# Optimization experiments

Measured on AMD Instinct MI355X. Metric: run time of the kernel, lower is better.

## Reference

```python
import jax, jax.numpy as jnp
import numpy as np

SEQ, B, IN, H = 512, 64, 1024, 1024

def _lstm_layer(x_seq, Wx, bx, Wh, bh):
    # x_seq: [S, B, D], Wx: [4H, D], Wh: [4H, H]
    h0 = jnp.zeros((x_seq.shape[1], Wh.shape[1]), x_seq.dtype)
    c0 = jnp.zeros_like(h0)
    def step(carry, x_t):
        h, c = carry
        z = x_t @ Wx.T + bx + h @ Wh.T + bh  # [B, 4H]
        i, f, g, o = jnp.split(z, 4, axis=1)
        c1 = jax.nn.sigmoid(f) * c + jax.nn.sigmoid(i) * jnp.tanh(g)
        h1 = jax.nn.sigmoid(o) * jnp.tanh(c1)
        return (h1, c1), h1
    _, hs = jax.lax.scan(step, (h0, c0), x_seq)
    return hs  # [S, B, H]

def setup_inputs() -> dict:
    key = jax.random.key(0)
    ks = jax.random.split(key, 9)
    s_in = 1.0 / np.sqrt(IN)
    s_h = 1.0 / np.sqrt(H)
    return {
        "x": jax.random.normal(ks[0], (SEQ, B, IN), jnp.float32),
        "Wx0": jax.random.uniform(ks[1], (4 * H, IN), jnp.float32, -s_in, s_in),
        "bx0": jax.random.uniform(ks[2], (4 * H,), jnp.float32, -s_in, s_in),
        "Wh0": jax.random.uniform(ks[3], (4 * H, H), jnp.float32, -s_h, s_h),
        "bh0": jax.random.uniform(ks[4], (4 * H,), jnp.float32, -s_h, s_h),
        "Wx1": jax.random.uniform(ks[5], (4 * H, H), jnp.float32, -s_h, s_h),
        "bx1": jax.random.uniform(ks[6], (4 * H,), jnp.float32, -s_h, s_h),
        "Wh1": jax.random.uniform(ks[7], (4 * H, H), jnp.float32, -s_h, s_h),
        "bh1": jax.random.uniform(ks[8], (4 * H,), jnp.float32, -s_h, s_h),
    }

def reference(x, Wx0, bx0, Wh0, bh0, Wx1, bx1, Wh1, bh1):
    # Two stacked unidirectional LSTM layers, zero initial states.
    h_seq0 = _lstm_layer(x, Wx0, bx0, Wh0, bh0)
    h_seq1 = _lstm_layer(h_seq0, Wx1, bx1, Wh1, bh1)
    return h_seq1  # [S, B, H] = stacked version of the torch list output
```

## Files before the change

kernel.cpp:

```cpp
#include <hip/hip_runtime.h>


#define SEQ   512
#define BATCH 64
#define HID   1024
#define NG    4096
#define KCAT  2048
#define F0_BASE 0
#define E0_IDX  8192
#define F1_BASE 16384
#define E1_IDX  24576

#define SMEM_BYTES 133504

typedef __attribute__((ext_vector_type(8))) _Float16 f16x8;
typedef __attribute__((ext_vector_type(4))) _Float16 f16x4;
typedef __attribute__((ext_vector_type(4))) float    f32x4;

__device__ __forceinline__ float sigm_f(float x){ return 1.f/(1.f + __expf(-x)); }
__device__ __forceinline__ float tanh_f(float x){
    float e = __expf(-2.f*fabsf(x));
    float r = (1.f - e)/(1.f + e);
    return copysignf(r, x);
}

__device__ __forceinline__ void store_h8(_Float16* p, f16x4 v){
    asm volatile("global_store_dwordx2 %0, %1, off sc0 sc1" :: "v"(p), "v"(v) : "memory");
}
__device__ __forceinline__ void drain_vmem(){
    asm volatile("s_waitcnt vmcnt(0)" ::: "memory");
}


__global__ void prep_w_kernel(const float* __restrict__ Wx, const float* __restrict__ Wh,
                              const float* __restrict__ bx, const float* __restrict__ bh,
                              _Float16* __restrict__ Wr, float* __restrict__ br){
    int p = blockIdx.x;
    int j = p >> 2, g = p & 3;
    int r = g*1024 + j;
    int k = threadIdx.x * 8;
    const float* s = (k < 1024) ? (Wx + (size_t)r*1024 + k)
                                : (Wh + (size_t)r*1024 + (k - 1024));
    float4 v0 = *reinterpret_cast<const float4*>(s);
    float4 v1 = *reinterpret_cast<const float4*>(s + 4);
    f16x8 o;
    o[0]=(_Float16)v0.x; o[1]=(_Float16)v0.y; o[2]=(_Float16)v0.z; o[3]=(_Float16)v0.w;
    o[4]=(_Float16)v1.x; o[5]=(_Float16)v1.y; o[6]=(_Float16)v1.z; o[7]=(_Float16)v1.w;
    *reinterpret_cast<f16x8*>(Wr + (size_t)p*KCAT + k) = o;
    if (threadIdx.x == 0) br[p] = bx[r] + bh[r];
}

__global__ void prep_x_kernel(const float* __restrict__ x, _Float16* xo){
    size_t i = ((size_t)blockIdx.x*256 + threadIdx.x) * 8;
    float4 v0 = *reinterpret_cast<const float4*>(x + i);
    float4 v1 = *reinterpret_cast<const float4*>(x + i + 4);
    f16x8 o;
    o[0]=(_Float16)v0.x; o[1]=(_Float16)v0.y; o[2]=(_Float16)v0.z; o[3]=(_Float16)v0.w;
    o[4]=(_Float16)v1.x; o[5]=(_Float16)v1.y; o[6]=(_Float16)v1.z; o[7]=(_Float16)v1.w;
    *reinterpret_cast<f16x8*>(xo + i) = o;
}

__global__ void init_misc_kernel(int* flags, _Float16* hz){
    int i = blockIdx.x*256 + threadIdx.x;
    flags[i] = 0;
    if (i < 16384){
        f16x4 z; z[0]=(_Float16)0.f; z[1]=(_Float16)0.f; z[2]=(_Float16)0.f; z[3]=(_Float16)0.f;
        *reinterpret_cast<f16x4*>(hz + (size_t)i*4) = z;
    }
}


__device__ __forceinline__ void wait_epoch_g(const int* flags, int eidx, int k, int rep){
    for(;;){
        int e = __hip_atomic_load(&flags[eidx + rep*32], __ATOMIC_RELAXED, __HIP_MEMORY_SCOPE_AGENT);
        if (e >= k) break;
        __builtin_amdgcn_s_sleep(2);
    }
    asm volatile("" ::: "memory");
}

__device__ __forceinline__ void aggregate_publish(int* flags, int base, int eidx,
                                                  int k, int lane){
    const int b = lane*4;
    for(;;){
        int a0 = __hip_atomic_load(&flags[base + (b+0)*32], __ATOMIC_RELAXED, __HIP_MEMORY_SCOPE_AGENT);
        int a1 = __hip_atomic_load(&flags[base + (b+1)*32], __ATOMIC_RELAXED, __HIP_MEMORY_SCOPE_AGENT);
        int a2 = __hip_atomic_load(&flags[base + (b+2)*32], __ATOMIC_RELAXED, __HIP_MEMORY_SCOPE_AGENT);
        int a3 = __hip_atomic_load(&flags[base + (b+3)*32], __ATOMIC_RELAXED, __HIP_MEMORY_SCOPE_AGENT);
        bool ok = (a0>=k) && (a1>=k) && (a2>=k) && (a3>=k);
        if (__all(ok)) break;
        __builtin_amdgcn_s_sleep(1);
    }
    asm volatile("" ::: "memory");
    if (lane < 8)
        __hip_atomic_store(&flags[eidx + lane*32], k, __ATOMIC_RELAXED, __HIP_MEMORY_SCOPE_AGENT);
}

__device__ __forceinline__ void lds_publish(int* e, int k){
    __hip_atomic_store(e, k, __ATOMIC_RELAXED, __HIP_MEMORY_SCOPE_WORKGROUP);
}
__device__ __forceinline__ void lds_wait(int* e, int k){
    while (__hip_atomic_load(e, __ATOMIC_RELAXED, __HIP_MEMORY_SCOPE_WORKGROUP) < k)
        __builtin_amdgcn_s_sleep(1);
    asm volatile("" ::: "memory");
}


__device__ __forceinline__ f32x4 mfma16(f16x8 a, f16x8 b, f32x4 c){
    return __builtin_amdgcn_mfma_f32_16x16x32_f16(a, b, c, 0, 0, 0);
}

__device__ __forceinline__ void gemm_pipe_ldsb(const _Float16* A, const char* wrow,
                                               int c0, int swz, f32x4* acc){
    f16x8 abuf[2][16];
    #pragma unroll
    for (int kk = 0; kk < 4; ++kk)
        #pragma unroll
        for (int m = 0; m < 4; ++m)
            abuf[0][kk*4+m] = *reinterpret_cast<const f16x8*>(A + kk*32 + m*16*1024);
    #pragma unroll
    for (int b = 0; b < 4; ++b){
        if (b < 3){
            #pragma unroll
            for (int kk = 0; kk < 4; ++kk)
                #pragma unroll
                for (int m = 0; m < 4; ++m)
                    abuf[(b+1)&1][kk*4+m] =
                        *reinterpret_cast<const f16x8*>(A + (b+1)*128 + kk*32 + m*16*1024);
        }
        #pragma unroll
        for (int kk = 0; kk < 4; ++kk){
            const int kg = b*4 + kk;
            f16x8 bb = *reinterpret_cast<const f16x8*>(wrow + ((c0 + kg*64) ^ swz));
            acc[0] = mfma16(abuf[b&1][kk*4+0], bb, acc[0]);
            acc[1] = mfma16(abuf[b&1][kk*4+1], bb, acc[1]);
            acc[2] = mfma16(abuf[b&1][kk*4+2], bb, acc[2]);
            acc[3] = mfma16(abuf[b&1][kk*4+3], bb, acc[3]);
        }
    }
}

__device__ __forceinline__ void gemm_pipe_gb(const _Float16* A, const _Float16* Wp,
                                             f32x4* acc){
    f16x8 abuf[2][16];
    #pragma unroll
    for (int kk = 0; kk < 4; ++kk)
        #pragma unroll
        for (int m = 0; m < 4; ++m)
            abuf[0][kk*4+m] = *reinterpret_cast<const f16x8*>(A + kk*32 + m*16*1024);
    #pragma unroll
    for (int b = 0; b < 4; ++b){
        if (b < 3){
            #pragma unroll
            for (int kk = 0; kk < 4; ++kk)
                #pragma unroll
                for (int m = 0; m < 4; ++m)
                    abuf[(b+1)&1][kk*4+m] =
                        *reinterpret_cast<const f16x8*>(A + (b+1)*128 + kk*32 + m*16*1024);
        }
        #pragma unroll
        for (int kk = 0; kk < 4; ++kk){
            const int kg = b*4 + kk;
            f16x8 bb = *reinterpret_cast<const f16x8*>(Wp + kg*32);
            acc[0] = mfma16(abuf[b&1][kk*4+0], bb, acc[0]);
            acc[1] = mfma16(abuf[b&1][kk*4+1], bb, acc[1]);
            acc[2] = mfma16(abuf[b&1][kk*4+2], bb, acc[2]);
            acc[3] = mfma16(abuf[b&1][kk*4+3], bb, acc[3]);
        }
    }
}

__device__ __forceinline__ void gemm_q_f32(const float* A, const _Float16* Wp, f32x4* acc){
    #pragma unroll 2
    for (int kk = 0; kk < 16; ++kk){
        f16x8 b = *reinterpret_cast<const f16x8*>(Wp + kk*32);
        f16x8 a[4];
        #pragma unroll
        for (int m = 0; m < 4; ++m){
            float4 u0 = *reinterpret_cast<const float4*>(A + kk*32 + (size_t)m*16*1024);
            float4 u1 = *reinterpret_cast<const float4*>(A + kk*32 + (size_t)m*16*1024 + 4);
            f16x8 v;
            v[0]=(_Float16)u0.x; v[1]=(_Float16)u0.y; v[2]=(_Float16)u0.z; v[3]=(_Float16)u0.w;
            v[4]=(_Float16)u1.x; v[5]=(_Float16)u1.y; v[6]=(_Float16)u1.z; v[7]=(_Float16)u1.w;
            a[m] = v;
        }
        acc[0] = mfma16(a[0], b, acc[0]);
        acc[1] = mfma16(a[1], b, acc[1]);
        acc[2] = mfma16(a[2], b, acc[2]);
        acc[3] = mfma16(a[3], b, acc[3]);
    }
}


__global__ __launch_bounds__(256, 1)
void lstm_persist(const _Float16* __restrict__ Wr0, const _Float16* __restrict__ Wr1,
                  const float* __restrict__ br0, const float* __restrict__ br1,
                  const _Float16* __restrict__ xbf, const float* __restrict__ xf32,
                  int use_xf16, const _Float16* __restrict__ hz,
                  _Float16* h0ring, _Float16* h1ring, float* out, int* flags){
    extern __shared__ char smem[];
    float (*accL)[4][64][17] = reinterpret_cast<float(*)[4][64][17]>(smem + 98304);
    int* ldsE = reinterpret_cast<int*>(smem + 133120);

    const int tid  = threadIdx.x;
    const int wg   = blockIdx.x;
    const int wv   = tid >> 6;
    const int lane = tid & 63;
    const int r    = lane & 15;
    const int q    = lane >> 4;
    const int p0   = wg * 16;
    const int rep  = wg & 7;
    const int swz  = (r & 7) << 4;

    for (int idx = tid; idx < 6144; idx += 256){
        int rr, cb; char* dst; const _Float16* s;
        if (idx < 2048){
            rr = idx >> 7;  cb = (idx & 127) << 4;
            s   = Wr0 + (size_t)(p0 + rr)*KCAT + 1024 + (cb >> 1);
            dst = smem + rr*2048 + (cb ^ ((rr & 7) << 4));
        } else {
            int j2 = idx - 2048;
            rr = j2 >> 8;  cb = (j2 & 255) << 4;
            s   = Wr1 + (size_t)(p0 + rr)*KCAT + (cb >> 1);
            dst = smem + 32768 + rr*4096 + (cb ^ ((rr & 7) << 4));
        }
        *reinterpret_cast<f16x8*>(dst) = *reinterpret_cast<const f16x8*>(s);
    }
    if (tid == 0) *ldsE = 0;
    __syncthreads();

    f32x4 cst = {0.f,0.f,0.f,0.f};
    f32x4 ho_keep = {0.f,0.f,0.f,0.f};
    f32x4 bias[4];
    {
        const float* bsrc = (wv == 0) ? br0 : br1;
        #pragma unroll
        for (int jj = 0; jj < 4; ++jj)
            bias[jj] = *reinterpret_cast<const f32x4*>(&bsrc[p0 + jj*4]);
    }

    const int kofs = (wv & 1)*512 + q*8;
    const int wcol = wv*512 + q*8;
    const char* w1row  = smem + 32768 + r*4096;
    const char* wh0row = smem + r*2048;
    const size_t BH = (size_t)BATCH*HID;

    for (int k = 0; k <= SEQ; ++k){
        f32x4 acc[4];
        #pragma unroll
        for (int m = 0; m < 4; ++m){ acc[m].x=0;acc[m].y=0;acc[m].z=0;acc[m].w=0; }

        if (wv < 2){
            if (k < SEQ){
                if (use_xf16)
                    gemm_pipe_gb(xbf + (size_t)k*BH + (size_t)r*HID + kofs,
                                 Wr0 + (size_t)(p0 + r)*KCAT + wcol, acc);
                else
                    gemm_q_f32(xf32 + (size_t)k*BH + (size_t)r*HID + kofs,
                               Wr0 + (size_t)(p0 + r)*KCAT + wcol, acc);
            }
        } else {
            if (k > 0){
                if (wv == 3){
                    if (wg == 0) aggregate_publish(flags, F0_BASE, E0_IDX, k, lane);
                    else         wait_epoch_g(flags, E0_IDX, k, rep);
                    lds_publish(ldsE, k);
                } else {
                    lds_wait(ldsE, k);
                }
            }
            if (k < SEQ){
                const _Float16* A0 = (k == 0) ? (hz + (size_t)r*HID + kofs)
                                              : (h0ring + (size_t)(k-1)*BH + (size_t)r*HID + kofs);
                gemm_pipe_ldsb(A0, wh0row, (wv-2)*1024 + q*16, swz, acc);
            }
        }

        #pragma unroll
        for (int mt = 0; mt < 4; ++mt)
            #pragma unroll
            for (int j = 0; j < 4; ++j)
                accL[0][wv][mt*16 + q*4 + j][r] = acc[mt][j];
        __syncthreads();

        if (wv == 0 && k < SEQ){
            f32x4 zz[4];
            #pragma unroll
            for (int jj = 0; jj < 4; ++jj) zz[jj] = bias[jj];
            #pragma unroll
            for (int w2 = 0; w2 < 4; ++w2)
                #pragma unroll
                for (int jj = 0; jj < 4; ++jj){
                    f32x4 a = *reinterpret_cast<const f32x4*>(&accL[0][w2][lane][jj*4]);
                    zz[jj].x += a.x; zz[jj].y += a.y; zz[jj].z += a.z; zz[jj].w += a.w;
                }
            f16x4 hv;
            #pragma unroll
            for (int jl = 0; jl < 4; ++jl){
                float ig = sigm_f(zz[jl].x), fg = sigm_f(zz[jl].y);
                float gg = tanh_f(zz[jl].z), og = sigm_f(zz[jl].w);
                float c = fg*cst[jl] + ig*gg;  cst[jl] = c;
                hv[jl] = (_Float16)(og * tanh_f(c));
            }
            store_h8(h0ring + ((size_t)k*BATCH + lane)*HID + wg*4, hv);
            drain_vmem();
            if (lane == 0)
                __hip_atomic_store(&flags[F0_BASE + wg*32], k + 1,
                                   __ATOMIC_RELAXED, __HIP_MEMORY_SCOPE_AGENT);
        }

        #pragma unroll
        for (int m = 0; m < 4; ++m){ acc[m].x=0;acc[m].y=0;acc[m].z=0;acc[m].w=0; }

        if (k >= 1){
            if (wv < 2){
                gemm_pipe_ldsb(h0ring + (size_t)(k-1)*BH + (size_t)r*HID + kofs,
                               w1row, wv*1024 + q*16, swz, acc);
            } else {
                if (k >= 2){
                    if (wg == 0 && wv == 2) aggregate_publish(flags, F1_BASE, E1_IDX, k-1, lane);
                    else                    wait_epoch_g(flags, E1_IDX, k-1, rep);
                }
                const _Float16* A1 = (k == 1) ? (hz + (size_t)r*HID + kofs)
                                              : (h1ring + (size_t)(k-2)*BH + (size_t)r*HID + kofs);
                gemm_pipe_ldsb(A1, w1row, wv*1024 + q*16, swz, acc);
            }
        }

        #pragma unroll
        for (int mt = 0; mt < 4; ++mt)
            #pragma unroll
            for (int j = 0; j < 4; ++j)
                accL[1][wv][mt*16 + q*4 + j][r] = acc[mt][j];
        __syncthreads();

        if (wv == 1 && k >= 1){
            const int t1 = k - 1;
            f32x4 zz[4];
            #pragma unroll
            for (int jj = 0; jj < 4; ++jj) zz[jj] = bias[jj];
            #pragma unroll
            for (int w2 = 0; w2 < 4; ++w2)
                #pragma unroll
                for (int jj = 0; jj < 4; ++jj){
                    f32x4 a = *reinterpret_cast<const f32x4*>(&accL[1][w2][lane][jj*4]);
                    zz[jj].x += a.x; zz[jj].y += a.y; zz[jj].z += a.z; zz[jj].w += a.w;
                }
            f16x4 hv; f32x4 ho;
            #pragma unroll
            for (int jl = 0; jl < 4; ++jl){
                float ig = sigm_f(zz[jl].x), fg = sigm_f(zz[jl].y);
                float gg = tanh_f(zz[jl].z), og = sigm_f(zz[jl].w);
                float c = fg*cst[jl] + ig*gg;  cst[jl] = c;
                float h = og * tanh_f(c);
                hv[jl] = (_Float16)h;  ho[jl] = h;
            }
            if (k < SEQ) store_h8(h1ring + ((size_t)t1*BATCH + lane)*HID + wg*4, hv);
            if (t1 < SEQ-1) *reinterpret_cast<f32x4*>(out + ((size_t)t1*BATCH + lane)*HID + wg*4) = ho;
            else            ho_keep = ho;
            drain_vmem();
            if (lane == 0)
                __hip_atomic_store(&flags[F1_BASE + wg*32], k,
                                   __ATOMIC_RELAXED, __HIP_MEMORY_SCOPE_AGENT);
        }
    }

    if (tid == 0)
        __hip_atomic_store(&flags[F0_BASE + wg*32], SEQ + 1,
                           __ATOMIC_RELAXED, __HIP_MEMORY_SCOPE_AGENT);
    if (wg == 0 && wv == 3) aggregate_publish(flags, F0_BASE, E0_IDX, SEQ + 1, lane);
    if (wv == 1){
        wait_epoch_g(flags, E0_IDX, SEQ + 1, rep);
        *reinterpret_cast<f32x4*>(out + ((size_t)(SEQ-1)*BATCH + lane)*HID + wg*4) = ho_keep;
    }
}


extern "C" void kernel_launch(void* const* d_in, const int* in_sizes, int n_in,
                              void* d_out, int out_size, void* d_ws, size_t ws_size,
                              hipStream_t stream){
    const float* x   = (const float*)d_in[0];
    const float* Wx0 = (const float*)d_in[1];
    const float* bx0 = (const float*)d_in[2];
    const float* Wh0 = (const float*)d_in[3];
    const float* bh0 = (const float*)d_in[4];
    const float* Wx1 = (const float*)d_in[5];
    const float* bx1 = (const float*)d_in[6];
    const float* Wh1 = (const float*)d_in[7];
    const float* bh1 = (const float*)d_in[8];
    float* out = (float*)d_out;
    char* ws = (char*)d_ws;

    size_t o = 0;
    _Float16* Wr0 = (_Float16*)(ws + o); o += (size_t)NG*KCAT*2;
    _Float16* Wr1 = (_Float16*)(ws + o); o += (size_t)NG*KCAT*2;
    float* br0 = (float*)(ws + o); o += 16384;
    float* br1 = (float*)(ws + o); o += 16384;
    _Float16* h1ring = (_Float16*)(ws + o); o += (size_t)SEQ*BATCH*HID*2;
    _Float16* hz     = (_Float16*)(ws + o); o += (size_t)BATCH*HID*2;
    int* flags = (int*)(ws + o); o += 131072;

    const size_t RING = (size_t)SEQ*BATCH*HID*2;
    _Float16 *xbf = nullptr, *h0ring;
    int use_xf16 = 0;
    if (ws_size >= o + 2*RING){
        xbf    = (_Float16*)(ws + o);  o += RING;  use_xf16 = 1;
        h0ring = (_Float16*)(ws + o);  o += RING;
    } else if (ws_size >= o + RING){
        xbf    = (_Float16*)(ws + o);  o += RING;  use_xf16 = 1;
        h0ring = (_Float16*)((char*)d_out + (size_t)64*1024*1024);
    } else {
        h0ring = (_Float16*)((char*)d_out + (size_t)64*1024*1024);
    }

    hipFuncSetAttribute((const void*)lstm_persist,
                        hipFuncAttributeMaxDynamicSharedMemorySize, SMEM_BYTES);

    prep_w_kernel<<<NG, 256, 0, stream>>>(Wx0, Wh0, bx0, bh0, Wr0, br0);
    prep_w_kernel<<<NG, 256, 0, stream>>>(Wx1, Wh1, bx1, bh1, Wr1, br1);
    if (use_xf16)
        prep_x_kernel<<<(SEQ*BATCH*HID)/(256*8), 256, 0, stream>>>(x, xbf);
    init_misc_kernel<<<128, 256, 0, stream>>>(flags, hz);
    lstm_persist<<<256, 256, SMEM_BYTES, stream>>>(Wr0, Wr1, br0, br1, xbf, x, use_xf16,
                                                   hz, h0ring, h1ring, out, flags);
}
```

Measured before the change: 8.843 ms.

## Add dedicated sync wave per block and replace syncthreads with counter barrier

```diff
diff --git a/kernel.cpp b/kernel.cpp
--- a/kernel.cpp
+++ b/kernel.cpp
@@ -11,7 +11,7 @@
 #define F1_BASE 16384
 #define E1_IDX  24576
 
-#define SMEM_BYTES 133504
+#define SMEM_BYTES 133184
 
 typedef __attribute__((ext_vector_type(8))) _Float16 f16x8;
 typedef __attribute__((ext_vector_type(4))) _Float16 f16x4;
@@ -70,38 +70,31 @@
 }
 
 
-__device__ __forceinline__ void wait_epoch_g(const int* flags, int eidx, int k, int rep){
-    for(;;){
-        int e = __hip_atomic_load(&flags[eidx + rep*32], __ATOMIC_RELAXED, __HIP_MEMORY_SCOPE_AGENT);
-        if (e >= k) break;
-        __builtin_amdgcn_s_sleep(2);
-    }
-    asm volatile("" ::: "memory");
-}
-
-__device__ __forceinline__ void aggregate_publish(int* flags, int base, int eidx,
-                                                  int k, int lane){
-    const int b = lane*4;
-    for(;;){
-        int a0 = __hip_atomic_load(&flags[base + (b+0)*32], __ATOMIC_RELAXED, __HIP_MEMORY_SCOPE_AGENT);
-        int a1 = __hip_atomic_load(&flags[base + (b+1)*32], __ATOMIC_RELAXED, __HIP_MEMORY_SCOPE_AGENT);
-        int a2 = __hip_atomic_load(&flags[base + (b+2)*32], __ATOMIC_RELAXED, __HIP_MEMORY_SCOPE_AGENT);
-        int a3 = __hip_atomic_load(&flags[base + (b+3)*32], __ATOMIC_RELAXED, __HIP_MEMORY_SCOPE_AGENT);
-        bool ok = (a0>=k) && (a1>=k) && (a2>=k) && (a3>=k);
-        if (__all(ok)) break;
-        __builtin_amdgcn_s_sleep(1);
-    }
-    asm volatile("" ::: "memory");
-    if (lane < 8)
-        __hip_atomic_store(&flags[eidx + lane*32], k, __ATOMIC_RELAXED, __HIP_MEMORY_SCOPE_AGENT);
-}
-
-__device__ __forceinline__ void lds_publish(int* e, int k){
-    __hip_atomic_store(e, k, __ATOMIC_RELAXED, __HIP_MEMORY_SCOPE_WORKGROUP);
-}
-__device__ __forceinline__ void lds_wait(int* e, int k){
+__device__ __forceinline__ int gload(const int* p){
+    return __hip_atomic_load(p, __ATOMIC_RELAXED, __HIP_MEMORY_SCOPE_AGENT);
+}
+__device__ __forceinline__ void gstore(int* p, int v){
+    __hip_atomic_store(p, v, __ATOMIC_RELAXED, __HIP_MEMORY_SCOPE_AGENT);
+}
+__device__ __forceinline__ void lstore(int* p, int v){
+    __hip_atomic_store(p, v, __ATOMIC_RELAXED, __HIP_MEMORY_SCOPE_WORKGROUP);
+}
+__device__ __forceinline__ void lds_wait(const int* e, int k){
     while (__hip_atomic_load(e, __ATOMIC_RELAXED, __HIP_MEMORY_SCOPE_WORKGROUP) < k)
         __builtin_amdgcn_s_sleep(1);
+    asm volatile("" ::: "memory");
+}
+__device__ __forceinline__ int wave_min(int v){
+    #pragma unroll
+    for (int off = 1; off < 64; off <<= 1)
+        v = min(v, __shfl_xor(v, off));
+    return v;
+}
+__device__ __forceinline__ void bar4(int* cnt, int target){
+    asm volatile("s_waitcnt lgkmcnt(0)" ::: "memory");
+    if ((threadIdx.x & 63) == 0)
+        __hip_atomic_fetch_add(cnt, 1, __ATOMIC_RELAXED, __HIP_MEMORY_SCOPE_WORKGROUP);
+    while (__hip_atomic_load(cnt, __ATOMIC_RELAXED, __HIP_MEMORY_SCOPE_WORKGROUP) < target) {}
     asm volatile("" ::: "memory");
 }
 
@@ -192,7 +185,7 @@
 }
 
 
-__global__ __launch_bounds__(256, 1)
+__global__ __launch_bounds__(320, 1)
 void lstm_persist(const _Float16* __restrict__ Wr0, const _Float16* __restrict__ Wr1,
                   const float* __restrict__ br0, const float* __restrict__ br1,
                   const _Float16* __restrict__ xbf, const float* __restrict__ xf32,
@@ -200,7 +193,9 @@
                   _Float16* h0ring, _Float16* h1ring, float* out, int* flags){
     extern __shared__ char smem[];
     float (*accL)[4][64][17] = reinterpret_cast<float(*)[4][64][17]>(smem + 98304);
-    int* ldsE = reinterpret_cast<int*>(smem + 133120);
+    int* ldsE0  = reinterpret_cast<int*>(smem + 133120);
+    int* ldsE1  = reinterpret_cast<int*>(smem + 133124);
+    int* barCnt = reinterpret_cast<int*>(smem + 133128);
 
     const int tid  = threadIdx.x;
     const int wg   = blockIdx.x;
@@ -209,10 +204,9 @@
     const int r    = lane & 15;
     const int q    = lane >> 4;
     const int p0   = wg * 16;
-    const int rep  = wg & 7;
     const int swz  = (r & 7) << 4;
 
-    for (int idx = tid; idx < 6144; idx += 256){
+    for (int idx = tid; idx < 6144; idx += 320){
         int rr, cb; char* dst; const _Float16* s;
         if (idx < 2048){
             rr = idx >> 7;  cb = (idx & 127) << 4;
@@ -226,8 +220,47 @@
         }
         *reinterpret_cast<f16x8*>(dst) = *reinterpret_cast<const f16x8*>(s);
     }
-    if (tid == 0) *ldsE = 0;
+    if (tid == 0){ *ldsE0 = 0; *ldsE1 = 0; *barCnt = 0; }
     __syncthreads();
+
+    if (wv == 4){
+        int e0 = 0, e1 = 0;
+        if (wg == 0){
+            for(;;){
+                int f0 = 0x7fffffff, f1 = 0x7fffffff;
+                #pragma unroll
+                for (int j = 0; j < 4; ++j){
+                    int i4 = lane*4 + j;
+                    f0 = min(f0, gload(&flags[F0_BASE + i4*32]));
+                    f1 = min(f1, gload(&flags[F1_BASE + i4*32]));
+                }
+                int g0 = wave_min(f0), g1 = wave_min(f1);
+                if (g0 > e0){
+                    if (lane < 32) gstore(&flags[E0_IDX + lane*32], g0);
+                    if (lane == 0) lstore(ldsE0, g0);
+                    e0 = g0;
+                }
+                if (g1 > e1){
+                    if (lane < 32) gstore(&flags[E1_IDX + lane*32], g1);
+                    if (lane == 0) lstore(ldsE1, g1);
+                    e1 = g1;
+                }
+                if (e1 >= SEQ) break;
+                __builtin_amdgcn_s_sleep(1);
+            }
+        } else {
+            const int ri = (wg & 31)*32;
+            for(;;){
+                int v0 = gload(&flags[E0_IDX + ri]);
+                int v1 = gload(&flags[E1_IDX + ri]);
+                if (v0 > e0){ if (lane == 0) lstore(ldsE0, v0); e0 = v0; }
+                if (v1 > e1){ if (lane == 0) lstore(ldsE1, v1); e1 = v1; }
+                if (e1 >= SEQ) break;
+                __builtin_amdgcn_s_sleep(1);
+            }
+        }
+        return;
+    }
 
     f32x4 cst = {0.f,0.f,0.f,0.f};
     f32x4 ho_keep = {0.f,0.f,0.f,0.f};
@@ -244,6 +277,7 @@
     const char* w1row  = smem + 32768 + r*4096;
     const char* wh0row = smem + r*2048;
     const size_t BH = (size_t)BATCH*HID;
+    int btgt = 4;
 
     for (int k = 0; k <= SEQ; ++k){
         f32x4 acc[4];
@@ -260,15 +294,7 @@
                                Wr0 + (size_t)(p0 + r)*KCAT + wcol, acc);
             }
         } else {
-            if (k > 0){
-                if (wv == 3){
-                    if (wg == 0) aggregate_publish(flags, F0_BASE, E0_IDX, k, lane);
-                    else         wait_epoch_g(flags, E0_IDX, k, rep);
-                    lds_publish(ldsE, k);
-                } else {
-                    lds_wait(ldsE, k);
-                }
-            }
+            if (k > 0) lds_wait(ldsE0, k);
             if (k < SEQ){
                 const _Float16* A0 = (k == 0) ? (hz + (size_t)r*HID + kofs)
                                               : (h0ring + (size_t)(k-1)*BH + (size_t)r*HID + kofs);
@@ -281,7 +307,7 @@
             #pragma unroll
             for (int j = 0; j < 4; ++j)
                 accL[0][wv][mt*16 + q*4 + j][r] = acc[mt][j];
-        __syncthreads();
+        bar4(barCnt, btgt); btgt += 4;
 
         if (wv == 0 && k < SEQ){
             f32x4 zz[4];
@@ -304,9 +330,7 @@
             }
             store_h8(h0ring + ((size_t)k*BATCH + lane)*HID + wg*4, hv);
             drain_vmem();
-            if (lane == 0)
-                __hip_atomic_store(&flags[F0_BASE + wg*32], k + 1,
-                                   __ATOMIC_RELAXED, __HIP_MEMORY_SCOPE_AGENT);
+            if (lane == 0) gstore(&flags[F0_BASE + wg*32], k + 1);
         }
 
         #pragma unroll
@@ -314,13 +338,11 @@
 
         if (k >= 1){
             if (wv < 2){
+                lds_wait(ldsE0, k);
                 gemm_pipe_ldsb(h0ring + (size_t)(k-1)*BH + (size_t)r*HID + kofs,
                                w1row, wv*1024 + q*16, swz, acc);
             } else {
-                if (k >= 2){
-                    if (wg == 0 && wv == 2) aggregate_publish(flags, F1_BASE, E1_IDX, k-1, lane);
-                    else                    wait_epoch_g(flags, E1_IDX, k-1, rep);
-                }
+                if (k >= 2) lds_wait(ldsE1, k-1);
                 const _Float16* A1 = (k == 1) ? (hz + (size_t)r*HID + kofs)
                                               : (h1ring + (size_t)(k-2)*BH + (size_t)r*HID + kofs);
                 gemm_pipe_ldsb(A1, w1row, wv*1024 + q*16, swz, acc);
@@ -332,7 +354,7 @@
             #pragma unroll
             for (int j = 0; j < 4; ++j)
                 accL[1][wv][mt*16 + q*4 + j][r] = acc[mt][j];
-        __syncthreads();
+        bar4(barCnt, btgt); btgt += 4;
 
         if (wv == 1 && k >= 1){
             const int t1 = k - 1;
@@ -359,18 +381,12 @@
             if (t1 < SEQ-1) *reinterpret_cast<f32x4*>(out + ((size_t)t1*BATCH + lane)*HID + wg*4) = ho;
             else            ho_keep = ho;
             drain_vmem();
-            if (lane == 0)
-                __hip_atomic_store(&flags[F1_BASE + wg*32], k,
-                                   __ATOMIC_RELAXED, __HIP_MEMORY_SCOPE_AGENT);
-        }
-    }
-
-    if (tid == 0)
-        __hip_atomic_store(&flags[F0_BASE + wg*32], SEQ + 1,
-                           __ATOMIC_RELAXED, __HIP_MEMORY_SCOPE_AGENT);
-    if (wg == 0 && wv == 3) aggregate_publish(flags, F0_BASE, E0_IDX, SEQ + 1, lane);
+            if (lane == 0) gstore(&flags[F1_BASE + wg*32], k);
+        }
+    }
+
     if (wv == 1){
-        wait_epoch_g(flags, E0_IDX, SEQ + 1, rep);
+        lds_wait(ldsE1, SEQ);
         *reinterpret_cast<f32x4*>(out + ((size_t)(SEQ-1)*BATCH + lane)*HID + wg*4) = ho_keep;
     }
 }
@@ -421,6 +437,6 @@
     if (use_xf16)
         prep_x_kernel<<<(SEQ*BATCH*HID)/(256*8), 256, 0, stream>>>(x, xbf);
     init_misc_kernel<<<128, 256, 0, stream>>>(flags, hz);
-    lstm_persist<<<256, 256, SMEM_BYTES, stream>>>(Wr0, Wr1, br0, br1, xbf, x, use_xf16,
+    lstm_persist<<<256, 320, SMEM_BYTES, stream>>>(Wr0, Wr1, br0, br1, xbf, x, use_xf16,
                                                    hz, h0ring, h1ring, out, flags);
 }
```

Measured after the change: 12.51 ms. 1.41x slower.

## Restructure epoch sync: more flag replicas, eager aggregation, simpler GEMM loads

Applied to the files above, without the earlier changes.

```diff
diff --git a/kernel.cpp b/kernel.cpp
--- a/kernel.cpp
+++ b/kernel.cpp
@@ -92,17 +92,8 @@
         __builtin_amdgcn_s_sleep(1);
     }
     asm volatile("" ::: "memory");
-    if (lane < 8)
+    if (lane < 32)
         __hip_atomic_store(&flags[eidx + lane*32], k, __ATOMIC_RELAXED, __HIP_MEMORY_SCOPE_AGENT);
-}
-
-__device__ __forceinline__ void lds_publish(int* e, int k){
-    __hip_atomic_store(e, k, __ATOMIC_RELAXED, __HIP_MEMORY_SCOPE_WORKGROUP);
-}
-__device__ __forceinline__ void lds_wait(int* e, int k){
-    while (__hip_atomic_load(e, __ATOMIC_RELAXED, __HIP_MEMORY_SCOPE_WORKGROUP) < k)
-        __builtin_amdgcn_s_sleep(1);
-    asm volatile("" ::: "memory");
 }
 
 
@@ -110,63 +101,65 @@
     return __builtin_amdgcn_mfma_f32_16x16x32_f16(a, b, c, 0, 0, 0);
 }
 
-__device__ __forceinline__ void gemm_pipe_ldsb(const _Float16* A, const char* wrow,
+__device__ __forceinline__ void gemm_half_ldsb(const _Float16* A, const char* wrow,
                                                int c0, int swz, f32x4* acc){
-    f16x8 abuf[2][16];
-    #pragma unroll
-    for (int kk = 0; kk < 4; ++kk)
+    f16x8 a[32];
+    #pragma unroll
+    for (int kk = 0; kk < 8; ++kk)
         #pragma unroll
         for (int m = 0; m < 4; ++m)
-            abuf[0][kk*4+m] = *reinterpret_cast<const f16x8*>(A + kk*32 + m*16*1024);
-    #pragma unroll
-    for (int b = 0; b < 4; ++b){
-        if (b < 3){
-            #pragma unroll
-            for (int kk = 0; kk < 4; ++kk)
-                #pragma unroll
-                for (int m = 0; m < 4; ++m)
-                    abuf[(b+1)&1][kk*4+m] =
-                        *reinterpret_cast<const f16x8*>(A + (b+1)*128 + kk*32 + m*16*1024);
-        }
-        #pragma unroll
-        for (int kk = 0; kk < 4; ++kk){
-            const int kg = b*4 + kk;
-            f16x8 bb = *reinterpret_cast<const f16x8*>(wrow + ((c0 + kg*64) ^ swz));
-            acc[0] = mfma16(abuf[b&1][kk*4+0], bb, acc[0]);
-            acc[1] = mfma16(abuf[b&1][kk*4+1], bb, acc[1]);
-            acc[2] = mfma16(abuf[b&1][kk*4+2], bb, acc[2]);
-            acc[3] = mfma16(abuf[b&1][kk*4+3], bb, acc[3]);
-        }
-    }
-}
-
-__device__ __forceinline__ void gemm_pipe_gb(const _Float16* A, const _Float16* Wp,
+            a[kk*4+m] = *reinterpret_cast<const f16x8*>(A + kk*32 + m*16*1024);
+    #pragma unroll
+    for (int kk = 0; kk < 8; ++kk){
+        f16x8 bb = *reinterpret_cast<const f16x8*>(wrow + ((c0 + kk*64) ^ swz));
+        acc[0] = mfma16(a[kk*4+0], bb, acc[0]);
+        acc[1] = mfma16(a[kk*4+1], bb, acc[1]);
+        acc[2] = mfma16(a[kk*4+2], bb, acc[2]);
+        acc[3] = mfma16(a[kk*4+3], bb, acc[3]);
+    }
+    #pragma unroll
+    for (int kk = 8; kk < 16; ++kk)
+        #pragma unroll
+        for (int m = 0; m < 4; ++m)
+            a[(kk-8)*4+m] = *reinterpret_cast<const f16x8*>(A + kk*32 + m*16*1024);
+    #pragma unroll
+    for (int kk = 8; kk < 16; ++kk){
+        f16x8 bb = *reinterpret_cast<const f16x8*>(wrow + ((c0 + kk*64) ^ swz));
+        acc[0] = mfma16(a[(kk-8)*4+0], bb, acc[0]);
+        acc[1] = mfma16(a[(kk-8)*4+1], bb, acc[1]);
+        acc[2] = mfma16(a[(kk-8)*4+2], bb, acc[2]);
+        acc[3] = mfma16(a[(kk-8)*4+3], bb, acc[3]);
+    }
+}
+
+__device__ __forceinline__ void gemm_half_gb(const _Float16* A, const _Float16* Wp,
                                              f32x4* acc){
-    f16x8 abuf[2][16];
-    #pragma unroll
-    for (int kk = 0; kk < 4; ++kk)
+    f16x8 a[32];
+    #pragma unroll
+    for (int kk = 0; kk < 8; ++kk)
         #pragma unroll
         for (int m = 0; m < 4; ++m)
-            abuf[0][kk*4+m] = *reinterpret_cast<const f16x8*>(A + kk*32 + m*16*1024);
-    #pragma unroll
-    for (int b = 0; b < 4; ++b){
-        if (b < 3){
-            #pragma unroll
-            for (int kk = 0; kk < 4; ++kk)
-                #pragma unroll
-                for (int m = 0; m < 4; ++m)
-                    abuf[(b+1)&1][kk*4+m] =
-                        *reinterpret_cast<const f16x8*>(A + (b+1)*128 + kk*32 + m*16*1024);
-        }
-        #pragma unroll
-        for (int kk = 0; kk < 4; ++kk){
-            const int kg = b*4 + kk;
-            f16x8 bb = *reinterpret_cast<const f16x8*>(Wp + kg*32);
-            acc[0] = mfma16(abuf[b&1][kk*4+0], bb, acc[0]);
-            acc[1] = mfma16(abuf[b&1][kk*4+1], bb, acc[1]);
-            acc[2] = mfma16(abuf[b&1][kk*4+2], bb, acc[2]);
-            acc[3] = mfma16(abuf[b&1][kk*4+3], bb, acc[3]);
-        }
+            a[kk*4+m] = *reinterpret_cast<const f16x8*>(A + kk*32 + m*16*1024);
+    #pragma unroll
+    for (int kk = 0; kk < 8; ++kk){
+        f16x8 bb = *reinterpret_cast<const f16x8*>(Wp + kk*32);
+        acc[0] = mfma16(a[kk*4+0], bb, acc[0]);
+        acc[1] = mfma16(a[kk*4+1], bb, acc[1]);
+        acc[2] = mfma16(a[kk*4+2], bb, acc[2]);
+        acc[3] = mfma16(a[kk*4+3], bb, acc[3]);
+    }
+    #pragma unroll
+    for (int kk = 8; kk < 16; ++kk)
+        #pragma unroll
+        for (int m = 0; m < 4; ++m)
+            a[(kk-8)*4+m] = *reinterpret_cast<const f16x8*>(A + kk*32 + m*16*1024);
+    #pragma unroll
+    for (int kk = 8; kk < 16; ++kk){
+        f16x8 bb = *reinterpret_cast<const f16x8*>(Wp + kk*32);
+        acc[0] = mfma16(a[(kk-8)*4+0], bb, acc[0]);
+        acc[1] = mfma16(a[(kk-8)*4+1], bb, acc[1]);
+        acc[2] = mfma16(a[(kk-8)*4+2], bb, acc[2]);
+        acc[3] = mfma16(a[(kk-8)*4+3], bb, acc[3]);
     }
 }
 
@@ -200,7 +193,6 @@
                   _Float16* h0ring, _Float16* h1ring, float* out, int* flags){
     extern __shared__ char smem[];
     float (*accL)[4][64][17] = reinterpret_cast<float(*)[4][64][17]>(smem + 98304);
-    int* ldsE = reinterpret_cast<int*>(smem + 133120);
 
     const int tid  = threadIdx.x;
     const int wg   = blockIdx.x;
@@ -209,7 +201,7 @@
     const int r    = lane & 15;
     const int q    = lane >> 4;
     const int p0   = wg * 16;
-    const int rep  = wg & 7;
+    const int rep  = wg & 31;
     const int swz  = (r & 7) << 4;
 
     for (int idx = tid; idx < 6144; idx += 256){
@@ -226,7 +218,6 @@
         }
         *reinterpret_cast<f16x8*>(dst) = *reinterpret_cast<const f16x8*>(s);
     }
-    if (tid == 0) *ldsE = 0;
     __syncthreads();
 
     f32x4 cst = {0.f,0.f,0.f,0.f};
@@ -253,26 +244,18 @@
         if (wv < 2){
             if (k < SEQ){
                 if (use_xf16)
-                    gemm_pipe_gb(xbf + (size_t)k*BH + (size_t)r*HID + kofs,
+                    gemm_half_gb(xbf + (size_t)k*BH + (size_t)r*HID + kofs,
                                  Wr0 + (size_t)(p0 + r)*KCAT + wcol, acc);
                 else
                     gemm_q_f32(xf32 + (size_t)k*BH + (size_t)r*HID + kofs,
                                Wr0 + (size_t)(p0 + r)*KCAT + wcol, acc);
             }
         } else {
-            if (k > 0){
-                if (wv == 3){
-                    if (wg == 0) aggregate_publish(flags, F0_BASE, E0_IDX, k, lane);
-                    else         wait_epoch_g(flags, E0_IDX, k, rep);
-                    lds_publish(ldsE, k);
-                } else {
-                    lds_wait(ldsE, k);
-                }
-            }
+            if (k > 0) wait_epoch_g(flags, E0_IDX, k, rep);
             if (k < SEQ){
                 const _Float16* A0 = (k == 0) ? (hz + (size_t)r*HID + kofs)
                                               : (h0ring + (size_t)(k-1)*BH + (size_t)r*HID + kofs);
-                gemm_pipe_ldsb(A0, wh0row, (wv-2)*1024 + q*16, swz, acc);
+                gemm_half_ldsb(A0, wh0row, (wv-2)*1024 + q*16, swz, acc);
             }
         }
 
@@ -282,6 +265,9 @@
             for (int j = 0; j < 4; ++j)
                 accL[0][wv][mt*16 + q*4 + j][r] = acc[mt][j];
         __syncthreads();
+
+        if (wg == 0 && wv == 3 && k < SEQ)
+            aggregate_publish(flags, F0_BASE, E0_IDX, k + 1, lane);
 
         if (wv == 0 && k < SEQ){
             f32x4 zz[4];
@@ -314,16 +300,13 @@
 
         if (k >= 1){
             if (wv < 2){
-                gemm_pipe_ldsb(h0ring + (size_t)(k-1)*BH + (size_t)r*HID + kofs,
+                gemm_half_ldsb(h0ring + (size_t)(k-1)*BH + (size_t)r*HID + kofs,
                                w1row, wv*1024 + q*16, swz, acc);
             } else {
-                if (k >= 2){
-                    if (wg == 0 && wv == 2) aggregate_publish(flags, F1_BASE, E1_IDX, k-1, lane);
-                    else                    wait_epoch_g(flags, E1_IDX, k-1, rep);
-                }
+                if (k >= 2) wait_epoch_g(flags, E1_IDX, k-1, rep);
                 const _Float16* A1 = (k == 1) ? (hz + (size_t)r*HID + kofs)
                                               : (h1ring + (size_t)(k-2)*BH + (size_t)r*HID + kofs);
-                gemm_pipe_ldsb(A1, w1row, wv*1024 + q*16, swz, acc);
+                gemm_half_ldsb(A1, w1row, wv*1024 + q*16, swz, acc);
             }
         }
 
@@ -333,6 +316,9 @@
             for (int j = 0; j < 4; ++j)
                 accL[1][wv][mt*16 + q*4 + j][r] = acc[mt][j];
         __syncthreads();
+
+        if (wg == 0 && wv == 2 && k >= 1)
+            aggregate_publish(flags, F1_BASE, E1_IDX, k, lane);
 
         if (wv == 1 && k >= 1){
             const int t1 = k - 1;
@@ -365,12 +351,8 @@
         }
     }
 
-    if (tid == 0)
-        __hip_atomic_store(&flags[F0_BASE + wg*32], SEQ + 1,
-                           __ATOMIC_RELAXED, __HIP_MEMORY_SCOPE_AGENT);
-    if (wg == 0 && wv == 3) aggregate_publish(flags, F0_BASE, E0_IDX, SEQ + 1, lane);
     if (wv == 1){
-        wait_epoch_g(flags, E0_IDX, SEQ + 1, rep);
+        wait_epoch_g(flags, E1_IDX, SEQ, rep);
         *reinterpret_cast<f32x4*>(out + ((size_t)(SEQ-1)*BATCH + lane)*HID + wg*4) = ho_keep;
     }
 }
```

After: 9.370 ms. 6.0% more time.
